# Kernel tuning notes

Hardware: AMD Instinct MI355X
Metric: run time of the kernel (lower is better)

The kernel has to match this reference:

```python
import jax, jax.numpy as jnp
import numpy as np

NUM_HEADS = 8
WS1, WS2 = 3, 5
SR = 8
RES = 56
DIM = 256


def _normalize(x, axis=-1, eps=1e-12):
    n = jnp.linalg.norm(x, axis=axis, keepdims=True)
    return x / jnp.maximum(n, eps)


def _unfold(img, ws):
    # img: (B, C, H, W) -> (B, C, ws*ws, H*W), torch nn.Unfold ordering
    B, C, H, W = img.shape
    p = ws // 2
    pad = jnp.pad(img, ((0, 0), (0, 0), (p, p), (p, p)))
    cols = jnp.stack([pad[:, :, i:i + H, j:j + W]
                      for i in range(ws) for j in range(ws)], axis=2)
    return cols.reshape(B, C, ws * ws, H * W)


def _local_mask(H, W, ws):
    # True where the unfolded window position falls on zero padding; shape (N, ws*ws)
    ones = jnp.ones((1, 1, H, W), jnp.float32)
    cols = _unfold(ones, ws)[0, 0]            # (ws*ws, N)
    return cols.T == 0                         # (N, ws*ws)


def _layernorm(x, g, b, eps=1e-5):
    mu = x.mean(-1, keepdims=True)
    var = ((x - mu) ** 2).mean(-1, keepdims=True)
    return (x - mu) * jax.lax.rsqrt(var + eps) * g + b


def setup_inputs() -> dict:
    key = jax.random.key(0)
    ks = jax.random.split(key, 8)
    C, B, N = DIM, 4, RES * RES
    hd = C // NUM_HEADS

    def nrm(k, shape, s=0.02):
        return jax.random.normal(k, shape, jnp.float32) * s

    return {
        "x": jax.random.normal(ks[0], (B, N, C), jnp.float32),
        "Wq": nrm(ks[1], (C, C)), "bq": jnp.zeros((C,), jnp.float32),
        "Wkv": nrm(ks[2], (C, 2 * C)), "bkv": jnp.zeros((2 * C,), jnp.float32),
        "Wsr": nrm(ks[3], (C, C)), "bsr": jnp.zeros((C,), jnp.float32),
        "ln_g": jnp.ones((C,), jnp.float32), "ln_b": jnp.zeros((C,), jnp.float32),
        "tok1": nrm(ks[4], (NUM_HEADS, hd, WS1 * WS1)),
        "bias1": jnp.zeros((NUM_HEADS, 1, WS1 * WS1), jnp.float32),
        "tok2": nrm(ks[5], (NUM_HEADS, hd, WS2 * WS2)),
        "bias2": jnp.zeros((NUM_HEADS, 1, WS2 * WS2), jnp.float32),
        "Wproj": nrm(ks[6], (C, C)), "bproj": jnp.zeros((C,), jnp.float32),
        "patch_size": 56,
    }


def reference(x, Wq, bq, Wkv, bkv, Wsr, bsr, ln_g, ln_b,
              tok1, bias1, tok2, bias2, Wproj, bproj, patch_size):
    H = W = int(patch_size)
    B, N, C = x.shape
    h = NUM_HEADS
    d = C // h
    l1, l2 = WS1 * WS1, WS2 * WS2

    # queries, cosine-normalized per head
    q = (x @ Wq + bq).reshape(B, N, h, d).transpose(0, 2, 1, 3)   # (B,h,N,d)
    qn = _normalize(q)

    # shared kv projection (torch computes it twice with identical result)
    kv = x @ Wkv + bkv
    k, v = kv[..., :C], kv[..., C:]
    kn = _normalize(k.reshape(B, N, h, d)).reshape(B, N, C)
    kv_img = jnp.concatenate([kn, v], axis=-1).transpose(0, 2, 1).reshape(B, 2 * C, H, W)

    def local_branch(ws):
        l = ws * ws
        cols = _unfold(kv_img, ws)                                # (B,2C,l,N)
        cols = cols.reshape(B, 2 * h, d, l, N).transpose(0, 1, 4, 2, 3)  # (B,2h,N,d,l)
        kl, vl = cols[:, :h], cols[:, h:]
        a = jnp.einsum('bhnd,bhndl->bhnl', qn, kl)
        a = jnp.where(_local_mask(H, W, ws)[None, None], -jnp.inf, a)
        return a, vl

    a1, vl1 = local_branch(WS1)
    a2, vl2 = local_branch(WS2)

    # pooled global branch
    x_img = x.transpose(0, 2, 1).reshape(B, C, H, W)
    x_sr = jnp.einsum('bchw,oc->bohw', x_img, Wsr.T.T) if False else jnp.einsum('bchw,co->bohw', x_img, Wsr) + bsr[None, :, None, None]
    x_sr = jax.nn.gelu(x_sr, approximate=False)
    pH, pW = H // SR, W // SR
    pooled = x_sr.reshape(B, C, pH, SR, pW, SR).mean(axis=(3, 5))  # adaptive avg pool
    P = pH * pW
    x_p = pooled.reshape(B, C, P).transpose(0, 2, 1)               # (B,P,C)
    x_p = _layernorm(x_p, ln_g, ln_b)
    kvp = (x_p @ Wkv + bkv).reshape(B, P, 2 * h, d).transpose(0, 2, 1, 3)
    kp, vp = kvp[:, :h], kvp[:, h:]
    ap = jnp.einsum('bhnd,bhpd->bhnp', qn, _normalize(kp))

    # joint softmax over both local windows and pooled tokens
    attn = jax.nn.softmax(jnp.concatenate([a1, a2, ap], axis=-1), axis=-1)
    s1 = attn[..., :l1]
    s2 = attn[..., l1:l1 + l2]
    sp = attn[..., l1 + l2:]

    x1 = jnp.einsum('bhnl,bhndl->bhnd',
                    jnp.einsum('bhnd,hdl->bhnl', qn, tok1) + bias1[None] + s1, vl1)
    x2 = jnp.einsum('bhnl,bhndl->bhnd',
                    jnp.einsum('bhnd,hdl->bhnl', qn, tok2) + bias2[None] + s2, vl2)
    xp = jnp.einsum('bhnp,bhpd->bhnd', sp, vp)

    out = (x1 + x2 + xp).transpose(0, 2, 1, 3).reshape(B, N, C)
    return out @ Wproj + bproj
```

## Files before the change

### kernel.cpp

```cpp
#include <hip/hip_runtime.h>
#include <hip/hip_bf16.h>

using bf16 = __hip_bfloat16;

#define B_  4
#define H_  56
#define W_  56
#define N_  3136
#define C_  256
#define NH  8
#define HD  32
#define P_  49
#define PH  7
#define TOKC 272
#define KS2  136
#define CPAD 80
#define VTH  60
#define VTW  64

typedef __attribute__((ext_vector_type(8))) short short8;
typedef __attribute__((ext_vector_type(4))) float f32x4;

union U8 { uint4 u; short8 s; };

__device__ __forceinline__ float bfu2f(ushort u) { return __uint_as_float((uint32_t)u << 16); }
__device__ __forceinline__ ushort f2bf_u(float f) {
    uint32_t u = __float_as_uint(f);
    uint32_t r = (u + 0x7FFFu + ((u >> 16) & 1u)) >> 16;
    return (ushort)r;
}
__device__ __forceinline__ uint32_t pk2(float a, float b) {
    return (uint32_t)f2bf_u(a) | ((uint32_t)f2bf_u(b) << 16);
}
__device__ __forceinline__ float lo16(uint32_t u) { return __uint_as_float(u << 16); }
__device__ __forceinline__ float hi16(uint32_t u) { return __uint_as_float(u & 0xffff0000u); }

__device__ __forceinline__ float half_reduce(float v) {
#pragma unroll
    for (int m = 16; m >= 1; m >>= 1) v += __shfl_xor(v, m);
    return v;
}

__device__ __forceinline__ float block_sum(float val, float* red) {
#pragma unroll
    for (int m = 32; m >= 1; m >>= 1) val += __shfl_xor(val, m);
    __syncthreads();
    if ((threadIdx.x & 63) == 0) red[threadIdx.x >> 6] = val;
    __syncthreads();
    return red[0] + red[1] + red[2] + red[3];
}

__global__ __launch_bounds__(256) void k_prep(
    const float* __restrict__ Wq, const float* __restrict__ Wkv,
    const float* __restrict__ Wsr, const float* __restrict__ Wproj,
    const float* __restrict__ tok1, const float* __restrict__ bias1,
    const float* __restrict__ tok2, const float* __restrict__ bias2,
    ushort* __restrict__ WT, ushort* __restrict__ WTp,
    ushort* __restrict__ TD, float* __restrict__ biasT,
    uint32_t* __restrict__ vT32, uint32_t* __restrict__ vpT32)
{
    const int gid = blockIdx.x * 256 + threadIdx.x;
    const int gs = gridDim.x * 256;
    for (int i = gid; i < 1024 * 256; i += gs) {
        int o = i >> 8, c = i & 255;
        float w = (o < 256) ? Wq[c * 256 + o]
                : (o < 768) ? Wkv[c * 512 + (o - 256)]
                            : Wsr[c * 256 + (o - 768)];
        WT[i] = f2bf_u(w);
    }
    for (int i = gid; i < 256 * 256; i += gs) {
        int o = i >> 8, c = i & 255;
        WTp[i] = f2bf_u(Wproj[c * 256 + o]);
    }
    for (int i = gid; i < 320 * 256; i += gs) {
        int j = i >> 8, k = i & 255;
        float val = 0.f;
        if (j < TOKC) {
            int h = j / 34, l = j % 34;
            if ((k >> 5) == h) {
                int d = k & 31;
                val = (l < 9) ? tok1[(h * HD + d) * 9 + l]
                              : tok2[(h * HD + d) * 25 + (l - 9)];
            }
        }
        TD[i] = f2bf_u(val);
    }
    for (int i = gid; i < 320; i += gs) {
        float bv = 0.f;
        if (i < TOKC) {
            int h = i / 34, l = i % 34;
            bv = (l < 9) ? bias1[h * 9 + l] : bias2[h * 25 + (l - 9)];
        }
        biasT[i] = bv;
    }
    const int nvt = B_ * 256 * VTH * VTW / 2;
    for (int i = gid; i < nvt; i += gs) vT32[i] = 0u;
    for (int i = gid; i < B_ * 256 * 32; i += gs) vpT32[i] = 0u;
}

__global__ __launch_bounds__(256) void k_gemm_in(
    const float* __restrict__ xf,
    const ushort* __restrict__ WT,
    const float* __restrict__ bq, const float* __restrict__ bkv,
    const float* __restrict__ bsr,
    ushort* __restrict__ qnu,
    ushort* __restrict__ knu, ushort* __restrict__ vT, ushort* __restrict__ srgu)
{
    const int r0 = blockIdx.x * 64;
    const int halfy = blockIdx.y;
    const int t = threadIdx.x;
    __shared__ __align__(16) ushort As[64 * 264];
    __shared__ __align__(16) ushort Bs[64 * 264];

#pragma unroll
    for (int i = 0; i < 8; i++) {
        int chunk = t + i * 256;
        int row = chunk >> 5, ks8 = (chunk & 31) * 8;
        const float* src = xf + (size_t)(r0 + row) * 256 + ks8;
        float4 f0 = *(const float4*)(src);
        float4 f1 = *(const float4*)(src + 4);
        uint4 o;
        o.x = pk2(f0.x, f0.y); o.y = pk2(f0.z, f0.w);
        o.z = pk2(f1.x, f1.y); o.w = pk2(f1.z, f1.w);
        *(uint4*)(As + row * 264 + ks8) = o;
    }
    __syncthreads();

    const int w = t >> 6, lane = t & 63;
    const int arow = w * 16 + (lane & 15);
    const int k0 = (lane >> 4) * 8;
    const int colq = lane & 15;
    const int rb = r0 + w * 16 + (lane >> 4) * 4;

    short8 areg[8];
#pragma unroll
    for (int kk = 0; kk < 8; kk++)
        areg[kk] = *(const short8*)(As + arow * 264 + kk * 32 + k0);

    for (int cc = 0; cc < 8; cc++) {
        const int cb = halfy * 512 + cc * 64;
        const int mode = cb >> 8;
        const int cm = cb & 255;

        __syncthreads();
#pragma unroll
        for (int i = 0; i < 8; i++) {
            int chunk = t + i * 256;
            int row = chunk >> 5, ks8 = (chunk & 31) * 8;
            *(uint4*)(Bs + row * 264 + ks8) =
                *(const uint4*)(WT + (size_t)(cb + row) * 256 + ks8);
        }
        __syncthreads();

        f32x4 acc[4];
#pragma unroll
        for (int ct = 0; ct < 4; ct++) acc[ct] = (f32x4){0.f, 0.f, 0.f, 0.f};
#pragma unroll
        for (int kk = 0; kk < 8; kk++) {
#pragma unroll
            for (int ct = 0; ct < 4; ct++) {
                short8 b = *(const short8*)(Bs + (ct * 16 + colq) * 264 + kk * 32 + k0);
                acc[ct] = __builtin_amdgcn_mfma_f32_16x16x32_bf16(areg[kk], b, acc[ct], 0, 0, 0);
            }
        }

        const float* bp = (mode == 0) ? bq : (mode == 1) ? bkv : (mode == 2) ? (bkv + 256) : bsr;
#pragma unroll
        for (int ct = 0; ct < 4; ct++) {
            float bv = bp[cm + ct * 16 + colq];
#pragma unroll
            for (int j = 0; j < 4; j++) acc[ct][j] += bv;
        }

        if (mode <= 1) {
#pragma unroll
            for (int hp = 0; hp < 2; hp++) {
#pragma unroll
                for (int j = 0; j < 4; j++) {
                    float ss = acc[2 * hp][j] * acc[2 * hp][j] + acc[2 * hp + 1][j] * acc[2 * hp + 1][j];
                    ss += __shfl_xor(ss, 1); ss += __shfl_xor(ss, 2);
                    ss += __shfl_xor(ss, 4); ss += __shfl_xor(ss, 8);
                    float inv = 1.0f / fmaxf(sqrtf(ss), 1e-12f);
                    acc[2 * hp][j] *= inv; acc[2 * hp + 1][j] *= inv;
                }
            }
        } else if (mode == 3) {
#pragma unroll
            for (int ct = 0; ct < 4; ct++)
#pragma unroll
                for (int j = 0; j < 4; j++) {
                    float s = acc[ct][j];
                    acc[ct][j] = 0.5f * s * (1.0f + erff(s * 0.70710678118654752f));
                }
        }

#pragma unroll
        for (int ct = 0; ct < 4; ct++) {
            int gcol = cm + ct * 16 + colq;
#pragma unroll
            for (int j = 0; j < 4; j++) {
                float vvv = acc[ct][j];
                size_t ro = (size_t)(rb + j);
                if (mode == 0)      qnu[ro * 256 + gcol] = f2bf_u(vvv);
                else if (mode == 1) knu[ro * 256 + gcol] = f2bf_u(vvv);
                else if (mode == 2) {
                    int bb = (int)(ro / N_), n = (int)(ro % N_);
                    int yy = n / W_, xx = n % W_;
                    vT[((size_t)(bb * 256 + gcol) * VTH + yy + 2) * VTW + xx + 2] = f2bf_u(vvv);
                } else {
                    srgu[ro * 256 + gcol] = f2bf_u(vvv);
                }
            }
        }
    }
}

template <int MODE>
__global__ __launch_bounds__(256) void k_gemm(
    const ushort* __restrict__ Abf,
    const ushort* __restrict__ WT,
    const float*  __restrict__ bias,
    float* __restrict__ dstF,
    ushort* __restrict__ dstT)
{
    const int r0 = blockIdx.x * 64;
    const int cb = blockIdx.y * 64;
    const int t = threadIdx.x;
    __shared__ __align__(16) ushort As[64 * 264];
    __shared__ __align__(16) ushort Bs[64 * 264];

#pragma unroll
    for (int i = 0; i < 8; i++) {
        int chunk = t + i * 256;
        int row = chunk >> 5, ks = (chunk & 31) * 8;
        *(uint4*)(As + row * 264 + ks) = *(const uint4*)(Abf + (size_t)(r0 + row) * 256 + ks);
        *(uint4*)(Bs + row * 264 + ks) = *(const uint4*)(WT + (size_t)(cb + row) * 256 + ks);
    }
    __syncthreads();

    const int w = t >> 6, lane = t & 63;
    const int arow = w * 16 + (lane & 15);
    const int k0 = (lane >> 4) * 8;
    f32x4 acc[4];
#pragma unroll
    for (int ct = 0; ct < 4; ct++) acc[ct] = (f32x4){0.f, 0.f, 0.f, 0.f};

#pragma unroll
    for (int kk = 0; kk < 8; kk++) {
        short8 a = *(const short8*)(As + arow * 264 + kk * 32 + k0);
#pragma unroll
        for (int ct = 0; ct < 4; ct++) {
            short8 b = *(const short8*)(Bs + (ct * 16 + (lane & 15)) * 264 + kk * 32 + k0);
            acc[ct] = __builtin_amdgcn_mfma_f32_16x16x32_bf16(a, b, acc[ct], 0, 0, 0);
        }
    }

    const int colq = lane & 15;
    const int rb = r0 + w * 16 + (lane >> 4) * 4;
#pragma unroll
    for (int ct = 0; ct < 4; ct++) {
        float bv = bias[cb + ct * 16 + colq];
#pragma unroll
        for (int j = 0; j < 4; j++) acc[ct][j] += bv;
    }

#pragma unroll
    for (int ct = 0; ct < 4; ct++) {
        int gcol = cb + ct * 16 + colq;
#pragma unroll
        for (int j = 0; j < 4; j++) {
            if (MODE == 4) {
                dstF[(size_t)(rb + j) * 256 + gcol] = acc[ct][j];
            } else {
                if (gcol < TOKC)
                    dstT[(size_t)(rb + j) * TOKC + gcol] = f2bf_u(acc[ct][j]);
            }
        }
    }
}

__global__ __launch_bounds__(256) void k_srt(
    const uint32_t* __restrict__ srgu32,
    const float* __restrict__ Wkv, const float* __restrict__ bkv,
    const float* __restrict__ ln_g, const float* __restrict__ ln_b,
    ushort* __restrict__ kpn_u, ushort* __restrict__ vpT)
{
    const int cell = blockIdx.x;
    const int b = cell / P_, p = cell % P_;
    const int py = p / PH, px = p % PH;
    const int t = threadIdx.x;
    const int ph = t >> 7, cp = t & 127;
    __shared__ float xp[C_];
    __shared__ float red[4];

    float sx = 0.f, sy = 0.f;
    for (int k = 0; k < 32; k++) {
        int pi = ph * 32 + k;
        int n = (py * 8 + (pi >> 3)) * W_ + px * 8 + (pi & 7);
        uint32_t u = srgu32[((size_t)b * N_ + n) * 128 + cp];
        sx += lo16(u); sy += hi16(u);
    }
    if (ph == 1) { xp[2 * cp] = sx; xp[2 * cp + 1] = sy; }
    __syncthreads();
    if (ph == 0) {
        xp[2 * cp]     = (xp[2 * cp] + sx) * (1.0f / 64.0f);
        xp[2 * cp + 1] = (xp[2 * cp + 1] + sy) * (1.0f / 64.0f);
    }
    __syncthreads();

    float acc = xp[t];
    float mean = block_sum(acc, red) * (1.0f / C_);
    float dv = acc - mean;
    float var = block_sum(dv * dv, red) * (1.0f / C_);
    float xpv = dv * rsqrtf(var + 1e-5f) * ln_g[t] + ln_b[t];
    __syncthreads();
    xp[t] = xpv;
    __syncthreads();

    float ak = bkv[t];
    float av = bkv[C_ + t];
    for (int c = 0; c < C_; c++) {
        float xv = xp[c];
        ak += xv * Wkv[c * 2 * C_ + t];
        av += xv * Wkv[c * 2 * C_ + C_ + t];
    }
    float nk = fmaxf(sqrtf(half_reduce(ak * ak)), 1e-12f);
    kpn_u[(size_t)cell * C_ + t] = f2bf_u(ak / nk);
    vpT[((size_t)b * 256 + t) * 64 + p] = f2bf_u(av);
}

__global__ __launch_bounds__(256) void k_qkav(
    const ushort* __restrict__ qnu,
    const uint32_t* __restrict__ knu,
    const ushort* __restrict__ kpnu,
    const ushort* __restrict__ tokcu,
    const ushort* __restrict__ vT,
    const ushort* __restrict__ vpT,
    ushort* __restrict__ preu)
{
    const int tile = blockIdx.x;
    const int b  = blockIdx.y >> 1;
    const int hs = blockIdx.y & 1;
    const int ty = tile / 14, tx = tile % 14;
    const int t = threadIdx.x;

    __shared__ __align__(16) ushort shmem[2 * 4 * 16 * CPAD];
    __shared__ ushort tokcS[16 * 136];
    ushort* ks = shmem;
    ushort* coefW = shmem;
    ushort* coefP = shmem + 4 * 16 * CPAD;

    uint32_t* ks32 = (uint32_t*)ks;
    for (int idx = t; idx < 64 * 32; idx += 256) {
        int r = idx >> 5, u2 = idx & 31;
        int gy = ty * 4 + (r >> 3) - 2, gx = tx * 4 + (r & 7) - 2;
        uint2 kv = make_uint2(0u, 0u);
        if (gy >= 0 && gy < H_ && gx >= 0 && gx < W_)
            kv = *reinterpret_cast<const uint2*>(
                knu + ((size_t)b * N_ + gy * W_ + gx) * 128 + hs * 64 + 2 * u2);
        ks32[r * (KS2 / 2) + 2 * u2]     = kv.x;
        ks32[r * (KS2 / 2) + 2 * u2 + 1] = kv.y;
    }
    {
        uint32_t* tokcS32 = (uint32_t*)tokcS;
        const uint32_t* tsrc = (const uint32_t*)tokcu;
        for (int idx = t; idx < 16 * 68; idx += 256) {
            int tk = idx / 68, d = idx % 68;
            size_t flat = (size_t)b * N_ + (ty * 4 + (tk >> 2)) * W_ + tx * 4 + (tk & 3);
            tokcS32[tk * 68 + d] = tsrc[flat * 136 + hs * 68 + d];
        }
    }
    __syncthreads();

    const int w = t >> 6, lane = t & 63;
    const int h = hs * 4 + w;
    const int col = lane & 15, kslc = lane >> 4;

    int r8[4], c8[4]; bool inb[4]; int pcl[4]; bool pval[4];
#pragma unroll
    for (int ct = 0; ct < 4; ct++) {
        int key = ct * 16 + col;
        r8[ct] = key >> 3; c8[ct] = key & 7;
        int gy = ty * 4 + r8[ct] - 2, gx = tx * 4 + c8[ct] - 2;
        inb[ct] = (gy >= 0) && (gy < H_) && (gx >= 0) && (gx < W_);
        pval[ct] = key < P_;
        pcl[ct] = pval[ct] ? key : (P_ - 1);
    }

    size_t aflat = (size_t)b * N_ + (ty * 4 + (col >> 2)) * W_ + tx * 4 + (col & 3);
    short8 a = *(const short8*)(qnu + aflat * 256 + h * 32 + kslc * 8);

    f32x4 aw[4], ap[4];
#pragma unroll
    for (int ct = 0; ct < 4; ct++) {
        short8 bw = *(const short8*)(ks + (ct * 16 + col) * KS2 + w * 32 + kslc * 8);
        aw[ct] = __builtin_amdgcn_mfma_f32_16x16x32_bf16(a, bw, (f32x4){0.f,0.f,0.f,0.f}, 0, 0, 0);
        short8 bp = *(const short8*)(kpnu + ((size_t)b * P_ + pcl[ct]) * 256 + h * 32 + kslc * 8);
        ap[ct] = __builtin_amdgcn_mfma_f32_16x16x32_bf16(a, bp, (f32x4){0.f,0.f,0.f,0.f}, 0, 0, 0);
    }

    __syncthreads();

#pragma unroll
    for (int j = 0; j < 4; j++) {
        float mj = -INFINITY;
#pragma unroll
        for (int ct = 0; ct < 4; ct++) {
            int dy = r8[ct] - kslc - 2, dx = c8[ct] - j - 2;
            bool win = inb[ct] && dy >= -2 && dy <= 2 && dx >= -2 && dx <= 2;
            if (win) mj = fmaxf(mj, aw[ct][j]);
            if (pval[ct]) mj = fmaxf(mj, ap[ct][j]);
        }
        mj = fmaxf(mj, __shfl_xor(mj, 1)); mj = fmaxf(mj, __shfl_xor(mj, 2));
        mj = fmaxf(mj, __shfl_xor(mj, 4)); mj = fmaxf(mj, __shfl_xor(mj, 8));
        float ej = 0.f;
        float ew[4], ep[4];
#pragma unroll
        for (int ct = 0; ct < 4; ct++) {
            int dy = r8[ct] - kslc - 2, dx = c8[ct] - j - 2;
            bool win = inb[ct] && dy >= -2 && dy <= 2 && dx >= -2 && dx <= 2;
            bool inner = dy >= -1 && dy <= 1 && dx >= -1 && dx <= 1;
            ew[ct] = win ? (inner ? 2.0f : 1.0f) * __expf(aw[ct][j] - mj) : 0.f;
            ep[ct] = pval[ct] ? __expf(ap[ct][j] - mj) : 0.f;
            ej += ew[ct] + ep[ct];
        }
        ej += __shfl_xor(ej, 1); ej += __shfl_xor(ej, 2);
        ej += __shfl_xor(ej, 4); ej += __shfl_xor(ej, 8);
        float sc = 1.0f / ej;
        const ushort* tokc_j = tokcS + (kslc * 4 + j) * 136 + w * 34;
        const int trow = (w * 16 + kslc * 4 + j) * CPAD;
#pragma unroll
        for (int ct = 0; ct < 4; ct++) {
            int dy = r8[ct] - kslc - 2, dx = c8[ct] - j - 2;
            float cw = 0.f;
            if (dy >= -2 && dy <= 2 && dx >= -2 && dx <= 2) {
                bool inner = dy >= -1 && dy <= 1 && dx >= -1 && dx <= 1;
                int l25 = (dy + 2) * 5 + (dx + 2);
                float tm = bfu2f(tokc_j[9 + l25]);
                if (inner) tm += bfu2f(tokc_j[(dy + 1) * 3 + (dx + 1)]);
                cw = ew[ct] * sc + tm;
            }
            coefW[trow + ct * 16 + col] = f2bf_u(cw);
            coefP[trow + ct * 16 + col] = f2bf_u(pval[ct] ? ep[ct] * sc : 0.f);
        }
    }
    __syncthreads();

    f32x4 accO[2];
    accO[0] = (f32x4){0.f,0.f,0.f,0.f};
    accO[1] = (f32x4){0.f,0.f,0.f,0.f};
#pragma unroll
    for (int kc = 0; kc < 2; kc++) {
        short8 aWf = *(const short8*)(coefW + (w * 16 + col) * CPAD + kc * 32 + kslc * 8);
        short8 aPf = *(const short8*)(coefP + (w * 16 + col) * CPAD + kc * 32 + kslc * 8);
#pragma unroll
        for (int ct = 0; ct < 2; ct++) {
            int chg = hs * 128 + w * 32 + ct * 16 + col;
            size_t vbase = (((size_t)(b * 256 + chg)) * VTH + ty * 4 + kc * 4 + kslc) * VTW + tx * 4;
            uint2 l0 = *(const uint2*)(vT + vbase);
            uint2 l1 = *(const uint2*)(vT + vbase + 4);
            U8 ub; ub.u = make_uint4(l0.x, l0.y, l1.x, l1.y);
            accO[ct] = __builtin_amdgcn_mfma_f32_16x16x32_bf16(aWf, ub.s, accO[ct], 0, 0, 0);
            short8 bPf = *(const short8*)(vpT + ((size_t)b * 256 + chg) * 64 + kc * 32 + kslc * 8);
            accO[ct] = __builtin_amdgcn_mfma_f32_16x16x32_bf16(aPf, bPf, accO[ct], 0, 0, 0);
        }
    }
#pragma unroll
    for (int ct = 0; ct < 2; ct++) {
        int chg = hs * 128 + w * 32 + ct * 16 + col;
#pragma unroll
        for (int j = 0; j < 4; j++) {
            size_t pflat = (size_t)b * N_ + (ty * 4 + kslc) * W_ + tx * 4 + j;
            preu[pflat * 256 + chg] = f2bf_u(accO[ct][j]);
        }
    }
}

extern "C" void kernel_launch(void* const* d_in, const int* in_sizes, int n_in,
                              void* d_out, int out_size, void* d_ws, size_t ws_size,
                              hipStream_t stream)
{
    (void)in_sizes; (void)n_in; (void)out_size; (void)ws_size;
    const float* x     = (const float*)d_in[0];
    const float* Wq    = (const float*)d_in[1];
    const float* bq    = (const float*)d_in[2];
    const float* Wkv   = (const float*)d_in[3];
    const float* bkv   = (const float*)d_in[4];
    const float* Wsr   = (const float*)d_in[5];
    const float* bsr   = (const float*)d_in[6];
    const float* ln_g  = (const float*)d_in[7];
    const float* ln_b  = (const float*)d_in[8];
    const float* tok1  = (const float*)d_in[9];
    const float* bias1 = (const float*)d_in[10];
    const float* tok2  = (const float*)d_in[11];
    const float* bias2 = (const float*)d_in[12];
    const float* Wproj = (const float*)d_in[13];
    const float* bproj = (const float*)d_in[14];
    float* out = (float*)d_out;

    const size_t nhalf = (size_t)B_ * N_ * 128;
    const size_t nvt   = (size_t)B_ * 256 * VTH * VTW;

    uint32_t* knu    = (uint32_t*)d_ws;
    uint32_t* srgu   = knu + nhalf;
    uint32_t* qnu32  = srgu + nhalf;
    ushort*   vTus   = (ushort*)(qnu32 + nhalf);
    ushort*   WTus   = vTus + nvt;
    ushort*   WTpus  = WTus + 1024 * 256;
    ushort*   TDus   = WTpus + 256 * 256;
    float*    biasT  = (float*)(TDus + 320 * 256);
    ushort*   vpTus  = (ushort*)(biasT + 320);
    ushort*   kpnuS  = vpTus + (size_t)B_ * 256 * 64;

    ushort* qnu   = (ushort*)qnu32;
    ushort* tokcu = (ushort*)d_out;

    k_prep<<<512, 256, 0, stream>>>(Wq, Wkv, Wsr, Wproj, tok1, bias1, tok2, bias2,
                                    WTus, WTpus, TDus, biasT,
                                    (uint32_t*)vTus, (uint32_t*)vpTus);
    k_gemm_in<<<dim3(196, 2), 256, 0, stream>>>(x, WTus, bq, bkv, bsr,
                                                qnu, (ushort*)knu, vTus, (ushort*)srgu);
    k_gemm<5><<<dim3(196, 5), 256, 0, stream>>>(qnu, TDus, biasT, nullptr, tokcu);
    k_srt<<<B_ * P_, 256, 0, stream>>>(srgu, Wkv, bkv, ln_g, ln_b, kpnuS, vpTus);
    k_qkav<<<dim3(196, B_ * 2), 256, 0, stream>>>(qnu, knu, kpnuS, tokcu,
                                                  vTus, vpTus, (ushort*)srgu);
    k_gemm<4><<<dim3(196, 4), 256, 0, stream>>>((ushort*)srgu, WTpus, bproj, out, nullptr);
}
```

Baseline: 114.7 us.

## Fuse token-coefficient GEMM into attention kernel and zero only vT padding border

Removes the separate k_gemm<5> launch that computed per-query token coefficients (qn·tok + bias) into a global buffer. k_qkav now computes them itself with three extra MFMAs per wave against the per-head TD slice and writes them straight into shared memory. k_prep also stops clearing the whole padded vT image and zeroes only the 2-pixel border, since the interior is overwritten later. This saves a kernel launch, a global round trip of the coefficient tensor, and most of the memset traffic, at the cost of a little more MFMA and TD-load work inside the attention kernel.

```diff
diff --git a/kernel.cpp b/kernel.cpp
--- a/kernel.cpp
+++ b/kernel.cpp
@@ -57,7 +57,7 @@
     const float* __restrict__ tok2, const float* __restrict__ bias2,
     ushort* __restrict__ WT, ushort* __restrict__ WTp,
     ushort* __restrict__ TD, float* __restrict__ biasT,
-    uint32_t* __restrict__ vT32, uint32_t* __restrict__ vpT32)
+    ushort* __restrict__ vT, uint32_t* __restrict__ vpT32)
 {
     const int gid = blockIdx.x * 256 + threadIdx.x;
     const int gs = gridDim.x * 256;
@@ -93,8 +93,14 @@
         }
         biasT[i] = bv;
     }
-    const int nvt = B_ * 256 * VTH * VTW / 2;
-    for (int i = gid; i < nvt; i += gs) vT32[i] = 0u;
+    const int nimg = B_ * 256;
+    for (int i = gid; i < nimg * 704; i += gs) {
+        int img = i / 704, c = i % 704;
+        int y, x;
+        if (c < 256) { int yi = c >> 6; y = (yi < 2) ? yi : yi + 56; x = c & 63; }
+        else { int cc = c - 256; y = 2 + cc / 8; int xx = cc % 8; x = (xx < 2) ? xx : xx + 56; }
+        vT[(size_t)img * VTH * VTW + y * VTW + x] = 0;
+    }
     for (int i = gid; i < B_ * 256 * 32; i += gs) vpT32[i] = 0u;
 }
 
@@ -215,13 +221,11 @@
     }
 }
 
-template <int MODE>
-__global__ __launch_bounds__(256) void k_gemm(
+__global__ __launch_bounds__(256) void k_gemm_proj(
     const ushort* __restrict__ Abf,
     const ushort* __restrict__ WT,
     const float*  __restrict__ bias,
-    float* __restrict__ dstF,
-    ushort* __restrict__ dstT)
+    float* __restrict__ dstF)
 {
     const int r0 = blockIdx.x * 64;
     const int cb = blockIdx.y * 64;
@@ -268,14 +272,8 @@
     for (int ct = 0; ct < 4; ct++) {
         int gcol = cb + ct * 16 + colq;
 #pragma unroll
-        for (int j = 0; j < 4; j++) {
-            if (MODE == 4) {
-                dstF[(size_t)(rb + j) * 256 + gcol] = acc[ct][j];
-            } else {
-                if (gcol < TOKC)
-                    dstT[(size_t)(rb + j) * TOKC + gcol] = f2bf_u(acc[ct][j]);
-            }
-        }
+        for (int j = 0; j < 4; j++)
+            dstF[(size_t)(rb + j) * 256 + gcol] = acc[ct][j];
     }
 }
 
@@ -333,7 +331,8 @@
     const ushort* __restrict__ qnu,
     const uint32_t* __restrict__ knu,
     const ushort* __restrict__ kpnu,
-    const ushort* __restrict__ tokcu,
+    const ushort* __restrict__ TD,
+    const float* __restrict__ biasT,
     const ushort* __restrict__ vT,
     const ushort* __restrict__ vpT,
     ushort* __restrict__ preu)
@@ -361,15 +360,6 @@
         ks32[r * (KS2 / 2) + 2 * u2]     = kv.x;
         ks32[r * (KS2 / 2) + 2 * u2 + 1] = kv.y;
     }
-    {
-        uint32_t* tokcS32 = (uint32_t*)tokcS;
-        const uint32_t* tsrc = (const uint32_t*)tokcu;
-        for (int idx = t; idx < 16 * 68; idx += 256) {
-            int tk = idx / 68, d = idx % 68;
-            size_t flat = (size_t)b * N_ + (ty * 4 + (tk >> 2)) * W_ + tx * 4 + (tk & 3);
-            tokcS32[tk * 68 + d] = tsrc[flat * 136 + hs * 68 + d];
-        }
-    }
     __syncthreads();
 
     const int w = t >> 6, lane = t & 63;
@@ -397,6 +387,23 @@
         aw[ct] = __builtin_amdgcn_mfma_f32_16x16x32_bf16(a, bw, (f32x4){0.f,0.f,0.f,0.f}, 0, 0, 0);
         short8 bp = *(const short8*)(kpnu + ((size_t)b * P_ + pcl[ct]) * 256 + h * 32 + kslc * 8);
         ap[ct] = __builtin_amdgcn_mfma_f32_16x16x32_bf16(a, bp, (f32x4){0.f,0.f,0.f,0.f}, 0, 0, 0);
+    }
+
+    f32x4 at[3];
+#pragma unroll
+    for (int ct = 0; ct < 3; ct++) {
+        short8 bt = *(const short8*)(TD + (size_t)(h * 34 + ct * 16 + col) * 256 + h * 32 + kslc * 8);
+        at[ct] = __builtin_amdgcn_mfma_f32_16x16x32_bf16(a, bt, (f32x4){0.f,0.f,0.f,0.f}, 0, 0, 0);
+    }
+#pragma unroll
+    for (int ct = 0; ct < 3; ct++) {
+        int l = ct * 16 + col;
+        if (l < 34) {
+            float bT = biasT[h * 34 + l];
+#pragma unroll
+            for (int j = 0; j < 4; j++)
+                tokcS[(kslc * 4 + j) * 136 + w * 34 + l] = f2bf_u(at[ct][j] + bT);
+        }
     }
 
     __syncthreads();
@@ -512,17 +519,15 @@
     ushort*   vpTus  = (ushort*)(biasT + 320);
     ushort*   kpnuS  = vpTus + (size_t)B_ * 256 * 64;
 
-    ushort* qnu   = (ushort*)qnu32;
-    ushort* tokcu = (ushort*)d_out;
+    ushort* qnu = (ushort*)qnu32;
 
     k_prep<<<512, 256, 0, stream>>>(Wq, Wkv, Wsr, Wproj, tok1, bias1, tok2, bias2,
                                     WTus, WTpus, TDus, biasT,
-                                    (uint32_t*)vTus, (uint32_t*)vpTus);
+                                    vTus, (uint32_t*)vpTus);
     k_gemm_in<<<dim3(196, 2), 256, 0, stream>>>(x, WTus, bq, bkv, bsr,
                                                 qnu, (ushort*)knu, vTus, (ushort*)srgu);
-    k_gemm<5><<<dim3(196, 5), 256, 0, stream>>>(qnu, TDus, biasT, nullptr, tokcu);
     k_srt<<<B_ * P_, 256, 0, stream>>>(srgu, Wkv, bkv, ln_g, ln_b, kpnuS, vpTus);
-    k_qkav<<<dim3(196, B_ * 2), 256, 0, stream>>>(qnu, knu, kpnuS, tokcu,
+    k_qkav<<<dim3(196, B_ * 2), 256, 0, stream>>>(qnu, knu, kpnuS, TDus, biasT,
                                                   vTus, vpTus, (ushort*)srgu);
-    k_gemm<4><<<dim3(196, 4), 256, 0, stream>>>((ushort*)srgu, WTpus, bproj, out, nullptr);
-}
+    k_gemm_proj<<<dim3(196, 4), 256, 0, stream>>>((ushort*)srgu, WTpus, bproj, out);
+}
```

Measured after the change: 106.4 us, median of 2. -7.2%, faster.
